# Kernel tuning notes

Hardware: AMD Instinct MI355X
Metric: run time of the kernel (lower is better)

The kernel has to match this reference:

```python
import jax, jax.numpy as jnp
import numpy as np

D = 128  # input_depth == output_depth
NUM_NODES_PATTERN = np.tile(np.array([32, 48, 64, 96], dtype=np.int64), 64)  # G=256 graphs


def _build_indices(nn_np):
    """Per pair-entry (row-major within each n_g x n_g block): global row node,
    global col node, graph id, diagonal mask; plus per-node graph id / size."""
    G = len(nn_np)
    offs = np.zeros(G, dtype=np.int64)
    offs[1:] = np.cumsum(nn_np)[:-1]
    rows_l, cols_l, g_l, diag_l = [], [], [], []
    for gi, (n, o) in enumerate(zip(nn_np, offs)):
        i = np.repeat(np.arange(n, dtype=np.int64), n)  # row index within block
        j = np.tile(np.arange(n, dtype=np.int64), n)    # col index within block
        rows_l.append(o + i)
        cols_l.append(o + j)
        g_l.append(np.full(n * n, gi, dtype=np.int64))
        diag_l.append(i == j)
    rows = np.concatenate(rows_l)
    cols = np.concatenate(cols_l)
    g_edge = np.concatenate(g_l)
    diag = np.concatenate(diag_l)
    g_node = np.repeat(np.arange(G, dtype=np.int64), nn_np)  # graph of each node
    n_node = np.repeat(nn_np, nn_np)                          # n_g of each node
    N = int(nn_np.sum())
    return rows, cols, g_edge, diag, g_node, n_node, N, G


def setup_inputs() -> dict:
    key = jax.random.key(0)
    nn_np = NUM_NODES_PATTERN
    E = int(np.sum(nn_np ** 2))  # 1,064,960 pair entries
    N = int(nn_np.sum())         # 15,360 nodes
    k1, k2, k3 = jax.random.split(key, 3)
    x = jax.random.normal(k1, (E, D), dtype=jnp.float32)
    coeffs = jax.random.normal(k2, (D, D, 5), dtype=jnp.float32) * float(np.sqrt(2.0) / (D + D))
    bias = jnp.zeros((1, D), dtype=jnp.float32)
    edges_index = jax.random.randint(k3, (2, E), 0, N, dtype=jnp.int64)  # unused by the layer
    num_nodes = jnp.asarray(nn_np)
    return {"x": x, "coeffs": coeffs, "bias": bias,
            "edges_index": edges_index, "num_nodes": num_nodes}


def reference(x, coeffs, bias, edges_index, num_nodes):
    # edges_index is unused, matching the original forward.
    nn_np = np.asarray(num_nodes)
    rows, cols, g_edge, diag, g_node, n_node, N, G = _build_indices(nn_np)
    seg = jax.ops.segment_sum
    diag_m = jnp.asarray(diag)[:, None].astype(x.dtype)  # [E,1]
    n = jnp.asarray(n_node).astype(x.dtype)[:, None]     # [N,1] block size per node

    op1 = seg(x * diag_m, jnp.asarray(rows), num_segments=N)          # diag part (unnormalized)
    op3 = seg(x, jnp.asarray(rows), num_segments=N) / n               # row sums / n
    op4 = seg(x, jnp.asarray(cols), num_segments=N) / n               # col sums / n
    diag_g = seg(x * diag_m, jnp.asarray(g_edge), num_segments=G)     # [G,d] trace per graph
    all_g = seg(x, jnp.asarray(g_edge), num_segments=G)               # [G,d] total sum per graph
    gn = jnp.asarray(g_node)
    op2 = diag_g[gn] / n                                              # trace broadcast / n
    op5 = all_g[gn] / (n * n)                                         # total broadcast / n^2

    ops = jnp.stack([op1, op2, op3, op4, op5], axis=2)                # [N, d, 5]
    out = jnp.einsum('dsb,ndb->ns', coeffs, ops) + bias               # [N, output_depth]
    return out
```

## Files before the change

kernel.cpp:

```cpp
#include <hip/hip_runtime.h>

#define D 128


template<int CTRL>
__device__ __forceinline__ float f_dpp_add(float v) {
    return v + __int_as_float(__builtin_amdgcn_update_dpp(
        0, __float_as_int(v), CTRL, 0xF, 0xF, true));
}

#define DPP_ROR8 0x128

__device__ __forceinline__ float f_xor16_sum(float v) {
#if __has_builtin(__builtin_amdgcn_permlane16_swap)
    typedef int v2i __attribute__((ext_vector_type(2)));
    v2i r = __builtin_amdgcn_permlane16_swap(__float_as_int(v), __float_as_int(v),
                                             false, false);
    return __int_as_float(r[0]) + __int_as_float(r[1]);
#else
    return v + __shfl_xor(v, 16);
#endif
}

__device__ __forceinline__ float f_xor32_sum(float v) {
#if __has_builtin(__builtin_amdgcn_permlane32_swap)
    typedef int v2i __attribute__((ext_vector_type(2)));
    v2i r = __builtin_amdgcn_permlane32_swap(__float_as_int(v), __float_as_int(v),
                                             false, false);
    return __int_as_float(r[0]) + __int_as_float(r[1]);
#else
    return v + __shfl_xor(v, 32);
#endif
}

__device__ __forceinline__ void f4add(float4& a, const float4& b) {
    a.x += b.x; a.y += b.y; a.z += b.z; a.w += b.w;
}

__device__ __forceinline__ void f4_jreduce_full(float4& a) {
    a.x = f_dpp_add<DPP_ROR8>(a.x);
    a.y = f_dpp_add<DPP_ROR8>(a.y);
    a.z = f_dpp_add<DPP_ROR8>(a.z);
    a.w = f_dpp_add<DPP_ROR8>(a.w);
    a.x = f_xor16_sum(a.x);
    a.y = f_xor16_sum(a.y);
    a.z = f_xor16_sum(a.z);
    a.w = f_xor16_sum(a.w);
    a.x = f_xor32_sum(a.x);
    a.y = f_xor32_sum(a.y);
    a.z = f_xor32_sum(a.z);
    a.w = f_xor32_sum(a.w);
}

template<int N>
__device__ __forceinline__ void run_class(const float* __restrict__ x,
                                          long ebase, int o, int gidx, int chunk,
                                          float* __restrict__ diagG,
                                          float* __restrict__ rowG,
                                          float* __restrict__ colG,
                                          float* __restrict__ trG,
                                          float* __restrict__ totG,
                                          float* __restrict__ colshare ,
                                          float* __restrict__ trshare  ,
                                          float* __restrict__ totshare ) {
    constexpr int CG = N / 8;
    const int tid  = threadIdx.x;
    const int l    = tid & 63;
    const int w    = tid >> 6;
    const int f4   = l & 7;
    const int jsub = l >> 3;
    const float invn = 1.0f / (float)N;

    for (int idx = tid; idx < N * 33; idx += 512) colshare[idx] = 0.f;
    if (tid < 32) { trshare[tid] = 0.f; totshare[tid] = 0.f; }
    __syncthreads();

    const float4* x4    = reinterpret_cast<const float4*>(x);
    float4*       diag4 = reinterpret_cast<float4*>(diagG);
    float4*       row4  = reinterpret_cast<float4*>(rowG);

    float4 colacc[CG];
#pragma unroll
    for (int cg = 0; cg < CG; ++cg) colacc[cg] = make_float4(0.f, 0.f, 0.f, 0.f);
    float4 tracc = make_float4(0.f, 0.f, 0.f, 0.f);

    for (int t = 0; t < N / 8; ++t) {
        const int i = w + 8 * t;
        const float4* rp = x4 + (ebase + (long)i * N + jsub) * 32 + chunk * 8 + f4;
        float4 racc = make_float4(0.f, 0.f, 0.f, 0.f);
#pragma unroll
        for (int cg = 0; cg < CG; ++cg) {
            float4 v = rp[cg * 256];
            f4add(racc, v);
            f4add(colacc[cg], v);
        }
        f4_jreduce_full(racc);
        if (l < 8) {
            float4 dv = x4[(ebase + (long)i * N + i) * 32 + chunk * 8 + f4];
            diag4[(long)(o + i) * 32 + chunk * 8 + f4] = dv;
            f4add(tracc, dv);
            float4 rv;
            rv.x = racc.x * invn; rv.y = racc.y * invn;
            rv.z = racc.z * invn; rv.w = racc.w * invn;
            row4[(long)(o + i) * 32 + chunk * 8 + f4] = rv;
        }
    }

#pragma unroll
    for (int cg = 0; cg < CG; ++cg) {
        float* cs = &colshare[(8 * cg + jsub) * 33 + f4 * 4];
        atomicAdd(cs + 0, colacc[cg].x);
        atomicAdd(cs + 1, colacc[cg].y);
        atomicAdd(cs + 2, colacc[cg].z);
        atomicAdd(cs + 3, colacc[cg].w);
    }
    if (l < 8) {
        float* ts = &trshare[f4 * 4];
        atomicAdd(ts + 0, tracc.x); atomicAdd(ts + 1, tracc.y);
        atomicAdd(ts + 2, tracc.z); atomicAdd(ts + 3, tracc.w);
    }
    __syncthreads();

    float tot = 0.f;
    for (int idx = tid; idx < N * 32; idx += 512) {
        const int col = idx >> 5;
        const int dd  = idx & 31;
        const float cv = colshare[col * 33 + dd];
        colG[(long)(o + col) * D + chunk * 32 + dd] = cv;
        tot += cv;
    }
    atomicAdd(&totshare[tid & 31], tot);
    __syncthreads();
    if (tid < 32) {
        trG [gidx * D + chunk * 32 + tid] = trshare[tid];
        totG[gidx * D + chunk * 32 + tid] = totshare[tid];
    }
}

__global__ __launch_bounds__(512) void k1_reduce(const float* __restrict__ x,
                                                 float* __restrict__ diagG,
                                                 float* __restrict__ rowG,
                                                 float* __restrict__ colG,
                                                 float* __restrict__ trG,
                                                 float* __restrict__ totG) {
    __shared__ float colshare[96 * 33];
    __shared__ float trshare[32];
    __shared__ float totshare[32];

    const int b  = blockIdx.x;
    const int bb = b & 255;
    const int k  = bb >> 2;
    const int chunk = bb & 3;

    if (b < 256) {
        run_class<96>(x, 16640L * k + 7424, 240 * k + 144, 4 * k + 3, chunk, diagG, rowG, colG, trG, totG, colshare, trshare, totshare);
    } else if (b < 512) {
        run_class<64>(x, 16640L * k + 3328, 240 * k + 80, 4 * k + 2, chunk, diagG, rowG, colG, trG, totG, colshare, trshare, totshare);
    } else if (b < 768) {
        run_class<48>(x, 16640L * k + 1024, 240 * k + 32, 4 * k + 1, chunk, diagG, rowG, colG, trG, totG, colshare, trshare, totshare);
    } else {
        run_class<32>(x, 16640L * k, 240 * k, 4 * k, chunk, diagG, rowG, colG, trG, totG, colshare, trshare, totshare);
    }
}

__global__ void k0_transpose(const float* __restrict__ coeffs, float* __restrict__ Wt) {
    int d = blockIdx.x;
    int s = threadIdx.x;
    const float* cp = coeffs + ((long)d * D + s) * 5;
#pragma unroll
    for (int b = 0; b < 5; ++b) Wt[b * (D * D) + d * D + s] = cp[b];
}

__global__ __launch_bounds__(128) void k2_pg(const float* __restrict__ trG,
                                             const float* __restrict__ totG,
                                             const float* __restrict__ Wt,
                                             const float* __restrict__ bias,
                                             float* __restrict__ pg) {
    __shared__ float tr[D], tt[D];
    const int ns_[4] = {32, 48, 64, 96};
    int g = blockIdx.x;
    int c = g & 3;
    float invn = 1.0f / (float)ns_[c];

    int s = threadIdx.x;
    tr[s] = trG[g * D + s] * invn;
    tt[s] = totG[g * D + s] * invn * invn;
    __syncthreads();

    const float* W1 = Wt + 1 * D * D;
    const float* W4 = Wt + 4 * D * D;
    float acc = 0.f;
#pragma unroll 4
    for (int dd = 0; dd < D; ++dd)
        acc += W1[dd * D + s] * tr[dd] + W4[dd * D + s] * tt[dd];
    pg[g * D + s] = bias[s] + acc;
}

__global__ __launch_bounds__(512) void k3_gemm(const float* __restrict__ diagG,
                                               const float* __restrict__ rowG,
                                               const float* __restrict__ colG,
                                               const float* __restrict__ Wt,
                                               const float* __restrict__ pg,
                                               float* __restrict__ out) {
    __shared__ __align__(16) float ash[3][64][D];
    __shared__ int gish[64];
    const int nd0 = blockIdx.x * 64;
    const int tid = threadIdx.x;

    const float4* diag4 = reinterpret_cast<const float4*>(diagG);
    const float4* row4  = reinterpret_cast<const float4*>(rowG);
    const float4* col4  = reinterpret_cast<const float4*>(colG);

    for (int idx = tid; idx < 64 * 32; idx += 512) {
        int nn = idx >> 5;
        int q  = idx & 31;
        int nd = nd0 + nn;
        int p  = nd / 240;
        int r  = nd - p * 240;
        int c, n;
        if (r < 32)       { c = 0; n = 32; }
        else if (r < 80)  { c = 1; n = 48; }
        else if (r < 144) { c = 2; n = 64; }
        else              { c = 3; n = 96; }
        float invn = 1.0f / (float)n;
        float4 dv = diag4[(long)nd * 32 + q];
        float4 rv = row4[(long)nd * 32 + q];
        float4 cv = col4[(long)nd * 32 + q];
        cv.x *= invn; cv.y *= invn; cv.z *= invn; cv.w *= invn;
        *reinterpret_cast<float4*>(&ash[0][nn][q * 4]) = dv;
        *reinterpret_cast<float4*>(&ash[1][nn][q * 4]) = rv;
        *reinterpret_cast<float4*>(&ash[2][nn][q * 4]) = cv;
        if (q == 0) gish[nn] = 4 * p + c;
    }
    __syncthreads();

    const int s4 = tid & 31;
    const int nq = tid >> 5;
    const float* W0 = Wt;
    const float* W2 = Wt + 2 * D * D;
    const float* W3 = Wt + 3 * D * D;

    float4 acc[4];
#pragma unroll
    for (int a = 0; a < 4; ++a) acc[a] = make_float4(0.f, 0.f, 0.f, 0.f);

    for (int d4 = 0; d4 < 32; ++d4) {
        float4 w0[4], w2[4], w3[4];
#pragma unroll
        for (int dd = 0; dd < 4; ++dd) {
            const int d = d4 * 4 + dd;
            w0[dd] = *reinterpret_cast<const float4*>(&W0[d * D + s4 * 4]);
            w2[dd] = *reinterpret_cast<const float4*>(&W2[d * D + s4 * 4]);
            w3[dd] = *reinterpret_cast<const float4*>(&W3[d * D + s4 * 4]);
        }
#pragma unroll
        for (int a = 0; a < 4; ++a) {
            const int nn = nq * 4 + a;
            float4 a0 = *reinterpret_cast<const float4*>(&ash[0][nn][d4 * 4]);
            float4 a1 = *reinterpret_cast<const float4*>(&ash[1][nn][d4 * 4]);
            float4 a2 = *reinterpret_cast<const float4*>(&ash[2][nn][d4 * 4]);
            const float* a0f = reinterpret_cast<const float*>(&a0);
            const float* a1f = reinterpret_cast<const float*>(&a1);
            const float* a2f = reinterpret_cast<const float*>(&a2);
#pragma unroll
            for (int dd = 0; dd < 4; ++dd) {
                acc[a].x += w0[dd].x * a0f[dd] + w2[dd].x * a1f[dd] + w3[dd].x * a2f[dd];
                acc[a].y += w0[dd].y * a0f[dd] + w2[dd].y * a1f[dd] + w3[dd].y * a2f[dd];
                acc[a].z += w0[dd].z * a0f[dd] + w2[dd].z * a1f[dd] + w3[dd].z * a2f[dd];
                acc[a].w += w0[dd].w * a0f[dd] + w2[dd].w * a1f[dd] + w3[dd].w * a2f[dd];
            }
        }
    }

#pragma unroll
    for (int a = 0; a < 4; ++a) {
        const int nn = nq * 4 + a;
        const int nd = nd0 + nn;
        const int g  = gish[nn];
        float4 pgv = *reinterpret_cast<const float4*>(&pg[g * D + s4 * 4]);
        float4 r_;
        r_.x = acc[a].x + pgv.x;
        r_.y = acc[a].y + pgv.y;
        r_.z = acc[a].z + pgv.z;
        r_.w = acc[a].w + pgv.w;
        *reinterpret_cast<float4*>(&out[(long)nd * D + s4 * 4]) = r_;
    }
}

extern "C" void kernel_launch(void* const* d_in, const int* in_sizes, int n_in,
                              void* d_out, int out_size, void* d_ws, size_t ws_size,
                              hipStream_t stream) {
    const float* x      = (const float*)d_in[0];
    const float* coeffs = (const float*)d_in[1];
    const float* bias   = (const float*)d_in[2];

    float* ws    = (float*)d_ws;
    float* Wt    = ws;
    float* diagG = Wt + 81920;
    float* rowG  = diagG + 1966080;
    float* colG  = rowG + 1966080;
    float* pg    = colG + 1966080;
    float* trG   = pg + 32768;
    float* totG  = trG + 32768;
    float* out   = (float*)d_out;

    k0_transpose<<<128, 128, 0, stream>>>(coeffs, Wt);
    k1_reduce<<<1024, 512, 0, stream>>>(x, diagG, rowG, colG, trG, totG);
    k2_pg<<<256, 128, 0, stream>>>(trG, totG, Wt, bias, pg);
    k3_gemm<<<240, 512, 0, stream>>>(diagG, rowG, colG, Wt, pg, out);
}
```

Measured before the change: 246.4 us.

## Split reduction by row slabs with partial column sums and combine kernel

Reworks the per-graph reduction so each block handles a 16-row slab of a graph across all 128 features, instead of one feature chunk over the whole graph. Per-slab column partials go through a double-buffered LDS tile and are written to global memory, then a new combine kernel sums slab partials into column sums, trace and totals. This drops the LDS float atomics and cross-lane row reductions and makes x reads contiguous per row. In exchange it adds a partial-sum buffer of about 34 MB in the workspace, an extra kernel launch, and more global traffic.

```diff
diff --git a/kernel.cpp b/kernel.cpp
--- a/kernel.cpp
+++ b/kernel.cpp
@@ -2,25 +2,6 @@
 
 #define D 128
 
-
-template<int CTRL>
-__device__ __forceinline__ float f_dpp_add(float v) {
-    return v + __int_as_float(__builtin_amdgcn_update_dpp(
-        0, __float_as_int(v), CTRL, 0xF, 0xF, true));
-}
-
-#define DPP_ROR8 0x128
-
-__device__ __forceinline__ float f_xor16_sum(float v) {
-#if __has_builtin(__builtin_amdgcn_permlane16_swap)
-    typedef int v2i __attribute__((ext_vector_type(2)));
-    v2i r = __builtin_amdgcn_permlane16_swap(__float_as_int(v), __float_as_int(v),
-                                             false, false);
-    return __int_as_float(r[0]) + __int_as_float(r[1]);
-#else
-    return v + __shfl_xor(v, 16);
-#endif
-}
 
 __device__ __forceinline__ float f_xor32_sum(float v) {
 #if __has_builtin(__builtin_amdgcn_permlane32_swap)
@@ -37,129 +18,154 @@
     a.x += b.x; a.y += b.y; a.z += b.z; a.w += b.w;
 }
 
-__device__ __forceinline__ void f4_jreduce_full(float4& a) {
-    a.x = f_dpp_add<DPP_ROR8>(a.x);
-    a.y = f_dpp_add<DPP_ROR8>(a.y);
-    a.z = f_dpp_add<DPP_ROR8>(a.z);
-    a.w = f_dpp_add<DPP_ROR8>(a.w);
-    a.x = f_xor16_sum(a.x);
-    a.y = f_xor16_sum(a.y);
-    a.z = f_xor16_sum(a.z);
-    a.w = f_xor16_sum(a.w);
+__device__ __forceinline__ void f4_xor32(float4& a) {
     a.x = f_xor32_sum(a.x);
     a.y = f_xor32_sum(a.y);
     a.z = f_xor32_sum(a.z);
     a.w = f_xor32_sum(a.w);
 }
 
+#define CP96 0L
+#define CP64 4718592L
+#define CP48 6815744L
+#define CP32 7995392L
+#define CP_TOTAL 8519680L
+
 template<int N>
 __device__ __forceinline__ void run_class(const float* __restrict__ x,
-                                          long ebase, int o, int gidx, int chunk,
+                                          long ebase, int o, int r0,
+                                          long cpbase, int slabIdx,
                                           float* __restrict__ diagG,
                                           float* __restrict__ rowG,
-                                          float* __restrict__ colG,
-                                          float* __restrict__ trG,
-                                          float* __restrict__ totG,
-                                          float* __restrict__ colshare ,
-                                          float* __restrict__ trshare  ,
-                                          float* __restrict__ totshare ) {
-    constexpr int CG = N / 8;
-    const int tid  = threadIdx.x;
-    const int l    = tid & 63;
-    const int w    = tid >> 6;
-    const int f4   = l & 7;
-    const int jsub = l >> 3;
+                                          float* __restrict__ colPart,
+                                          float* __restrict__ trPart,
+                                          float4* __restrict__ coltile ,
+                                          float* __restrict__ red      ) {
+    const int tid = threadIdx.x;
+    const int l   = tid & 63;
+    const int w   = tid >> 6;
+    const int s   = l & 31;
+    const int rh  = l >> 5;
+    const int row = r0 + 2 * w + rh;
     const float invn = 1.0f / (float)N;
 
-    for (int idx = tid; idx < N * 33; idx += 512) colshare[idx] = 0.f;
-    if (tid < 32) { trshare[tid] = 0.f; totshare[tid] = 0.f; }
+    const float4* x4 = reinterpret_cast<const float4*>(x);
+    const float4* p  = x4 + (ebase + (long)row * N) * 32 + s;
+
+    float4 racc = {0,0,0,0};
+    float4 dv   = {0,0,0,0};
+
+    int buf = 0;
+    for (int mt = 0; mt < N; mt += 8, buf ^= 1) {
+#pragma unroll
+        for (int m = 0; m < 8; ++m) {
+            const int col = mt + m;
+            float4 v = p[(long)col * 32];
+            f4add(racc, v);
+            if (col == row) dv = v;
+            float4 u = v;
+            f4_xor32(u);
+            if (l < 32) coltile[((buf * 8 + m) * 8 + w) * 32 + s] = u;
+        }
+        __syncthreads();
+        const float* ct = reinterpret_cast<const float*>(coltile) + buf * 8192;
+#pragma unroll
+        for (int it = 0; it < 2; ++it) {
+            const int item = tid + it * 512;
+            const int cc = item >> 7;
+            const int dd = item & 127;
+            float a = 0.f;
+#pragma unroll
+            for (int w2 = 0; w2 < 8; ++w2) a += ct[(cc * 8 + w2) * 128 + dd];
+            colPart[cpbase + (long)(mt + cc) * 128 + dd] = a;
+        }
+    }
+
+    float4* diag4 = reinterpret_cast<float4*>(diagG);
+    float4* row4  = reinterpret_cast<float4*>(rowG);
+    diag4[(long)(o + row) * 32 + s] = dv;
+    float4 rv;
+    rv.x = racc.x * invn; rv.y = racc.y * invn;
+    rv.z = racc.z * invn; rv.w = racc.w * invn;
+    row4[(long)(o + row) * 32 + s] = rv;
+
+    float4 td = dv;
+    f4_xor32(td);
+    if (l < 32) reinterpret_cast<float4*>(red)[w * 32 + s] = td;
     __syncthreads();
-
-    const float4* x4    = reinterpret_cast<const float4*>(x);
-    float4*       diag4 = reinterpret_cast<float4*>(diagG);
-    float4*       row4  = reinterpret_cast<float4*>(rowG);
-
-    float4 colacc[CG];
-#pragma unroll
-    for (int cg = 0; cg < CG; ++cg) colacc[cg] = make_float4(0.f, 0.f, 0.f, 0.f);
-    float4 tracc = make_float4(0.f, 0.f, 0.f, 0.f);
-
-    for (int t = 0; t < N / 8; ++t) {
-        const int i = w + 8 * t;
-        const float4* rp = x4 + (ebase + (long)i * N + jsub) * 32 + chunk * 8 + f4;
-        float4 racc = make_float4(0.f, 0.f, 0.f, 0.f);
-#pragma unroll
-        for (int cg = 0; cg < CG; ++cg) {
-            float4 v = rp[cg * 256];
-            f4add(racc, v);
-            f4add(colacc[cg], v);
-        }
-        f4_jreduce_full(racc);
-        if (l < 8) {
-            float4 dv = x4[(ebase + (long)i * N + i) * 32 + chunk * 8 + f4];
-            diag4[(long)(o + i) * 32 + chunk * 8 + f4] = dv;
-            f4add(tracc, dv);
-            float4 rv;
-            rv.x = racc.x * invn; rv.y = racc.y * invn;
-            rv.z = racc.z * invn; rv.w = racc.w * invn;
-            row4[(long)(o + i) * 32 + chunk * 8 + f4] = rv;
-        }
-    }
-
-#pragma unroll
-    for (int cg = 0; cg < CG; ++cg) {
-        float* cs = &colshare[(8 * cg + jsub) * 33 + f4 * 4];
-        atomicAdd(cs + 0, colacc[cg].x);
-        atomicAdd(cs + 1, colacc[cg].y);
-        atomicAdd(cs + 2, colacc[cg].z);
-        atomicAdd(cs + 3, colacc[cg].w);
-    }
-    if (l < 8) {
-        float* ts = &trshare[f4 * 4];
-        atomicAdd(ts + 0, tracc.x); atomicAdd(ts + 1, tracc.y);
-        atomicAdd(ts + 2, tracc.z); atomicAdd(ts + 3, tracc.w);
-    }
-    __syncthreads();
-
-    float tot = 0.f;
-    for (int idx = tid; idx < N * 32; idx += 512) {
-        const int col = idx >> 5;
-        const int dd  = idx & 31;
-        const float cv = colshare[col * 33 + dd];
-        colG[(long)(o + col) * D + chunk * 32 + dd] = cv;
-        tot += cv;
-    }
-    atomicAdd(&totshare[tid & 31], tot);
-    __syncthreads();
-    if (tid < 32) {
-        trG [gidx * D + chunk * 32 + tid] = trshare[tid];
-        totG[gidx * D + chunk * 32 + tid] = totshare[tid];
+    if (tid < 128) {
+        float a = 0.f;
+#pragma unroll
+        for (int w2 = 0; w2 < 8; ++w2) a += red[w2 * 128 + tid];
+        trPart[(long)slabIdx * 128 + tid] = a;
     }
 }
 
 __global__ __launch_bounds__(512) void k1_reduce(const float* __restrict__ x,
                                                  float* __restrict__ diagG,
                                                  float* __restrict__ rowG,
-                                                 float* __restrict__ colG,
-                                                 float* __restrict__ trG,
-                                                 float* __restrict__ totG) {
-    __shared__ float colshare[96 * 33];
-    __shared__ float trshare[32];
-    __shared__ float totshare[32];
-
-    const int b  = blockIdx.x;
-    const int bb = b & 255;
-    const int k  = bb >> 2;
-    const int chunk = bb & 3;
-
-    if (b < 256) {
-        run_class<96>(x, 16640L * k + 7424, 240 * k + 144, 4 * k + 3, chunk, diagG, rowG, colG, trG, totG, colshare, trshare, totshare);
-    } else if (b < 512) {
-        run_class<64>(x, 16640L * k + 3328, 240 * k + 80, 4 * k + 2, chunk, diagG, rowG, colG, trG, totG, colshare, trshare, totshare);
-    } else if (b < 768) {
-        run_class<48>(x, 16640L * k + 1024, 240 * k + 32, 4 * k + 1, chunk, diagG, rowG, colG, trG, totG, colshare, trshare, totshare);
+                                                 float* __restrict__ colPart,
+                                                 float* __restrict__ trPart) {
+    __shared__ __align__(16) float4 coltile[2 * 8 * 8 * 32];
+    __shared__ float red[8 * 128];
+
+    const int b = blockIdx.x;
+    if (b < 384) {
+        const int k = b / 6, rb = b - 6 * k;
+        run_class<96>(x, 16640L * k + 7424, 240 * k + 144, rb * 16,
+                      CP96 + (long)b * 12288, b, diagG, rowG, colPart, trPart, coltile, red);
+    } else if (b < 640) {
+        const int bb = b - 384, k = bb >> 2, rb = bb & 3;
+        run_class<64>(x, 16640L * k + 3328, 240 * k + 80, rb * 16,
+                      CP64 + (long)bb * 8192, b, diagG, rowG, colPart, trPart, coltile, red);
+    } else if (b < 832) {
+        const int bb = b - 640, k = bb / 3, rb = bb - 3 * k;
+        run_class<48>(x, 16640L * k + 1024, 240 * k + 32, rb * 16,
+                      CP48 + (long)bb * 6144, b, diagG, rowG, colPart, trPart, coltile, red);
     } else {
-        run_class<32>(x, 16640L * k, 240 * k, 4 * k, chunk, diagG, rowG, colG, trG, totG, colshare, trshare, totshare);
+        const int bb = b - 832, k = bb >> 1, rb = bb & 1;
+        run_class<32>(x, 16640L * k, 240 * k, rb * 16,
+                      CP32 + (long)bb * 4096, b, diagG, rowG, colPart, trPart, coltile, red);
+    }
+}
+
+__global__ __launch_bounds__(256) void k1b_combine(const float* __restrict__ colPart,
+                                                   const float* __restrict__ trPart,
+                                                   float* __restrict__ colG,
+                                                   float* __restrict__ trG,
+                                                   float* __restrict__ totG) {
+    __shared__ float lds[256];
+    const int g = blockIdx.x;
+    const int p = g >> 2, c = g & 3;
+    const int ns_[4] = {32, 48, 64, 96};
+    const int np_[4] = {0, 32, 80, 144};
+    const int n  = ns_[c];
+    const int o  = 240 * p + np_[c];
+    const int SC = n / 16;
+    long base; int sb;
+    if (c == 3)      { base = CP96 + (long)(6 * p) * 12288; sb = 6 * p; }
+    else if (c == 2) { base = CP64 + (long)(4 * p) * 8192;  sb = 384 + 4 * p; }
+    else if (c == 1) { base = CP48 + (long)(3 * p) * 6144;  sb = 640 + 3 * p; }
+    else             { base = CP32 + (long)(2 * p) * 4096;  sb = 832 + 2 * p; }
+    const long ssz = (long)n * 128;
+
+    const int tid = threadIdx.x;
+    float tot = 0.f;
+    for (int item = tid; item < n * 128; item += 256) {
+        float a = 0.f;
+        for (int sl = 0; sl < SC; ++sl) a += colPart[base + sl * ssz + item];
+        const int j  = item >> 7;
+        const int dd = item & 127;
+        colG[(long)(o + j) * D + dd] = a;
+        tot += a;
+    }
+    lds[tid] = tot;
+    __syncthreads();
+    if (tid < 128) {
+        totG[g * D + tid] = lds[tid] + lds[tid + 128];
+        float t = 0.f;
+        for (int sl = 0; sl < SC; ++sl) t += trPart[(long)(sb + sl) * 128 + tid];
+        trG[g * D + tid] = t;
     }
 }
 
@@ -294,18 +300,22 @@
     const float* coeffs = (const float*)d_in[1];
     const float* bias   = (const float*)d_in[2];
 
-    float* ws    = (float*)d_ws;
-    float* Wt    = ws;
-    float* diagG = Wt + 81920;
-    float* rowG  = diagG + 1966080;
-    float* colG  = rowG + 1966080;
-    float* pg    = colG + 1966080;
-    float* trG   = pg + 32768;
-    float* totG  = trG + 32768;
-    float* out   = (float*)d_out;
+    float* ws      = (float*)d_ws;
+    float* Wt      = ws;
+    float* diagG   = Wt + 81920;
+    float* rowG    = diagG + 1966080;
+    float* colG    = rowG + 1966080;
+    float* pg      = colG + 1966080;
+    float* trG     = pg + 32768;
+    float* totG    = trG + 32768;
+    float* colPart = totG + 32768;
+    float* trPart  = colPart + CP_TOTAL;
+
+    float* out = (float*)d_out;
 
     k0_transpose<<<128, 128, 0, stream>>>(coeffs, Wt);
-    k1_reduce<<<1024, 512, 0, stream>>>(x, diagG, rowG, colG, trG, totG);
+    k1_reduce<<<960, 512, 0, stream>>>(x, diagG, rowG, colPart, trPart);
+    k1b_combine<<<256, 256, 0, stream>>>(colPart, trPart, colG, trG, totG);
     k2_pg<<<256, 128, 0, stream>>>(trG, totG, Wt, bias, pg);
     k3_gemm<<<240, 512, 0, stream>>>(diagG, rowG, colG, Wt, pg, out);
 }
```

Measured after the change: 360.3 us. 1.46x slower.
